# Performance work log

Hardware: AMD Instinct MI355X
Metric: run time of the kernel (lower is better)

## Reference

```python
import jax, jax.numpy as jnp
import numpy as np
from jax import lax

# VGG16 conv configuration: (in_ch, out_ch) for 13 3x3 convs, blocks [2,2,3,3,3]
CONV_CFG = [(3,64),(64,64),(64,128),(128,128),(128,256),(256,256),(256,256),(256,512),(512,512),(512,512),(512,512),(512,512),(512,512)]
FC_CFG = [(512*7*7,4096),(4096,4096),(4096,1000)]
BLOCKS = [2,2,3,3,3]

def setup_inputs() -> dict:
    key = jax.random.key(0)
    ks = jax.random.split(key, 40)
    d = {"x": jax.random.normal(ks[0], (16,3,224,224), jnp.float32)}
    for i, (cin, cout) in enumerate(CONV_CFG):
        std = (2.0 / (cin * 9)) ** 0.5  # He init keeps 13-deep ReLU chain stable
        d[f"w{i+1}"] = jax.random.normal(ks[1+i], (cout, cin, 3, 3), jnp.float32) * std
        d[f"b{i+1}"] = jnp.zeros((cout,), jnp.float32)
    for j, (fin, fout) in enumerate(FC_CFG):
        std = (2.0 / fin) ** 0.5
        d[f"fw{j+1}"] = jax.random.normal(ks[20+j], (fin, fout), jnp.float32) * std
        d[f"fb{j+1}"] = jnp.zeros((fout,), jnp.float32)
    d["patch_location_tensor"] = jax.random.randint(ks[30], (16, 2), 0, 200)
    d["p_height"] = 16
    d["p_width"] = 16
    return d

def _conv_relu(x, w, b):
    # 3x3 conv, stride 1, SAME padding (pad=1), NCHW, followed by ReLU
    y = lax.conv_general_dilated(x, w, (1, 1), 'SAME', dimension_numbers=('NCHW', 'OIHW', 'NCHW'))
    return jax.nn.relu(y + b[None, :, None, None])

def _maxpool2(x):
    return lax.reduce_window(x, -jnp.inf, lax.max, (1, 1, 2, 2), (1, 1, 2, 2), 'VALID')

def reference(x, w1, b1, w2, b2, w3, b3, w4, b4, w5, b5, w6, b6, w7, b7, w8, b8, w9, b9, w10, b10, w11, b11, w12, b12, w13, b13, fw1, fb1, fw2, fb2, fw3, fb3, patch_location_tensor, p_height, p_width):
    # The incremental modules patch-update cached full-model activations; the net
    # result equals a dense VGG16 forward on x. patch_location_tensor / p_height /
    # p_width only control which region is recomputed, not the output values.
    ws = [w1, w2, w3, w4, w5, w6, w7, w8, w9, w10, w11, w12, w13]
    bs = [b1, b2, b3, b4, b5, b6, b7, b8, b9, b10, b11, b12, b13]
    h = x
    k = 0
    for n in BLOCKS:
        for _ in range(n):
            h = _conv_relu(h, ws[k], bs[k])
            k += 1
        h = _maxpool2(h)
    h = h.reshape(h.shape[0], -1)  # [B, 25088]
    h = jax.nn.relu(h @ fw1 + fb1)
    h = jax.nn.relu(h @ fw2 + fb2)
    return h @ fw3 + fb3  # [B, 1000]
```

## Files before the change

### kernel.cpp

```cpp
#include <hip/hip_runtime.h>
#include <hip/hip_bf16.h>

typedef __hip_bfloat16 bf16;
typedef __attribute__((ext_vector_type(4))) short s16x4;
typedef __attribute__((ext_vector_type(8))) short short8;
typedef __attribute__((ext_vector_type(8))) __bf16 bf16x8;
typedef __attribute__((ext_vector_type(4))) float f32x4;

__device__ __forceinline__ float s2f(short s) {
  return __builtin_bit_cast(float, (unsigned)((unsigned short)s) << 16);
}
__device__ __forceinline__ short f2s(float f) {
  return __builtin_bit_cast(short, __float2bfloat16(f));
}

__device__ __forceinline__ void gl16(const bf16* g, bf16* l) {
  __builtin_amdgcn_global_load_lds(
      (const __attribute__((address_space(1))) void*)g,
      (__attribute__((address_space(3))) void*)l, 16, 0, 0);
}

__global__ void zerofill(float* p, int n) {
  int i = blockIdx.x * 256 + threadIdx.x;
  if (i < n) p[i] = 0.f;
}

__global__ __launch_bounds__(256) void conv1_first(
    const float* __restrict__ x, const float* __restrict__ w,
    const float* __restrict__ b, bf16* __restrict__ out) {
  __shared__ float it[3][18][18];
  __shared__ float wl2[27 * 64];
  __shared__ float bl[64];
  const int tid = threadIdx.x;
  const int n = blockIdx.z;
  const int h0 = blockIdx.y * 16, w0 = blockIdx.x * 16;
  for (int i = tid; i < 1728; i += 256) {
    int jj = i >> 6, co = i & 63;
    wl2[i] = w[co * 27 + jj];
  }
  if (tid < 64) bl[tid] = b[tid];
  for (int i = tid; i < 972; i += 256) {
    int ci = i / 324; int r = i - ci * 324; int ty = r / 18, tx = r - ty * 18;
    int hh = h0 - 1 + ty, ww = w0 - 1 + tx;
    float v = 0.f;
    if (hh >= 0 && hh < 224 && ww >= 0 && ww < 224)
      v = x[((long)n * 3 + ci) * 50176 + hh * 224 + ww];
    it[ci][ty][tx] = v;
  }
  __syncthreads();
  const int ty = tid >> 4, tx = tid & 15;
  long ob = (((long)n * 224 + h0 + ty) * 224 + (w0 + tx)) * 64;
  for (int cog = 0; cog < 4; ++cog) {
    f32x4 a4[4];
    #pragma unroll
    for (int q = 0; q < 4; ++q) a4[q] = *(const f32x4*)&bl[cog * 16 + q * 4];
    #pragma unroll
    for (int jj = 0; jj < 27; ++jj) {
      const int ci = jj / 9, r = jj - ci * 9, kh = r / 3, kw = r - kh * 3;
      float v = it[ci][ty + kh][tx + kw];
      const f32x4* wp4 = (const f32x4*)&wl2[jj * 64 + cog * 16];
      #pragma unroll
      for (int q = 0; q < 4; ++q) a4[q] += v * wp4[q];
    }
    short8 s0, s1;
    #pragma unroll
    for (int u = 0; u < 4; ++u) {
      s0[u] = f2s(fmaxf(a4[0][u], 0.f));
      s0[4 + u] = f2s(fmaxf(a4[1][u], 0.f));
      s1[u] = f2s(fmaxf(a4[2][u], 0.f));
      s1[4 + u] = f2s(fmaxf(a4[3][u], 0.f));
    }
    *(short8*)(out + ob + cog * 16) = s0;
    *(short8*)(out + ob + cog * 16 + 8) = s1;
  }
}

struct RepackMeta {
  const float* src[12];
  long dstOff[12];
  int cinM1[12];
  int cshift[12];
  int cout[12];
};

__global__ __launch_bounds__(256) void repack_all(RepackMeta m, bf16* __restrict__ blob) {
  const int li = blockIdx.y;
  const int co = blockIdx.x;
  if (co >= m.cout[li]) return;
  const int cs = m.cshift[li];
  const int cinM1 = m.cinM1[li];
  const int K = 9 << cs;
  const float* src = m.src[li] + (long)co * (cinM1 + 1) * 9;
  bf16* dst = blob + m.dstOff[li] + (long)co * K;
  for (int k = threadIdx.x; k < K; k += 256) {
    int pos = k >> cs;
    int ci = k & cinM1;
    dst[k] = __float2bfloat16(src[ci * 9 + pos]);
  }
}

template <int BM, int BN, int WM, int WN, int SPLITK>
__global__ __launch_bounds__(WM* WN * 64) void conv_gemm(
    const bf16* __restrict__ in, const bf16* __restrict__ wp,
    const float* __restrict__ bias, bf16* __restrict__ out,
    float* __restrict__ pout, const bf16* __restrict__ zp,
    int Cin, int cshift, int Cout, int H, int W, int NHW) {
  constexpr int NT = WM * WN * 64;
  constexpr int IA = BM * 8 / NT;
  constexpr int IB = BN * 8 / NT;
  __shared__ bf16 lA[BM * 64];
  __shared__ bf16 lB[BN * 64];
  const int tid = threadIdx.x;
  const int lane = tid & 63, wv = tid >> 6;
  const int wr = wv / WN, wc = wv % WN;

  const int gx = gridDim.x;
  const int nwg = gx * gridDim.y;
  const int fid = blockIdx.y * gx + blockIdx.x;
  const int q = nwg >> 3, r = nwg & 7;
  const int xcd = fid & 7, idx = fid >> 3;
  const int swz = (xcd < r ? xcd * (q + 1) : r * (q + 1) + (xcd - r) * q) + idx;
  const int p0 = (swz % gx) * BM;
  const int co0 = (swz / gx) * BN;

  const int K = 9 << cshift;
  const int HW = H * W;
  const int colx = ((tid & 7) ^ ((tid >> 3) & 7)) * 8;

  int baseA[IA]; short hA[IA], wA[IA];
  #pragma unroll
  for (int i = 0; i < IA; ++i) {
    int rr = i * (NT / 8) + (tid >> 3);
    int p = p0 + rr;
    if (p < NHW) {
      int n = p / HW; int rem = p - n * HW; int h = rem / W; int w_ = rem - h * W;
      hA[i] = (short)h; wA[i] = (short)w_;
      baseA[i] = ((n * H + h) * W + w_) * Cin;
    } else { hA[i] = -9999; wA[i] = -9999; baseA[i] = 0; }
  }

  f32x4 acc[4][4];
  #pragma unroll
  for (int m = 0; m < 4; ++m)
    #pragma unroll
    for (int n2 = 0; n2 < 4; ++n2) acc[m][n2] = (f32x4){0.f, 0.f, 0.f, 0.f};

  const int Kper = K / SPLITK;
  const int kBeg = (SPLITK > 1) ? (int)blockIdx.z * Kper : 0;
  const int kEnd = kBeg + Kper;

  const bf16* srcB[IB];
  #pragma unroll
  for (int i = 0; i < IB; ++i) {
    int col = i * (NT / 8) + (tid >> 3);
    srcB[i] = wp + (long)(co0 + col) * K + kBeg + colx;
  }

  int kk = kBeg;
  while (kk < kEnd) {
    const int pos = kk >> cshift;
    const int dh = pos / 3 - 1, dw = pos - (pos / 3) * 3 - 1;
    int posEnd = (pos + 1) << cshift;
    if (posEnd > kEnd) posEnd = kEnd;
    const bf16* srcA[IA];
    {
      const int doff = (dh * W + dw) * Cin + (kk & (Cin - 1)) + colx;
      #pragma unroll
      for (int i = 0; i < IA; ++i) {
        int hh = hA[i] + dh, ww = wA[i] + dw;
        bool ok = (hh >= 0) & (hh < H) & (ww >= 0) & (ww < W);
        srcA[i] = ok ? (in + baseA[i] + doff) : (zp + colx);
      }
    }
    for (; kk < posEnd; kk += 64) {
      __syncthreads();
      #pragma unroll
      for (int i = 0; i < IA; ++i) {
        gl16(srcA[i], lA + i * (NT * 8) + wv * 512);
        srcA[i] += 64;
      }
      #pragma unroll
      for (int i = 0; i < IB; ++i) {
        gl16(srcB[i], lB + i * (NT * 8) + wv * 512);
        srcB[i] += 64;
      }
      __syncthreads();
      #pragma unroll
      for (int ks = 0; ks < 2; ++ks) {
        const int kb = ks * 64 + (lane >> 4) * 16;
        bf16x8 af[4], bfv[4];
        #pragma unroll
        for (int m = 0; m < 4; ++m) {
          int rr = wr * 64 + m * 16 + (lane & 15);
          af[m] = *(const bf16x8*)((const char*)lA + rr * 128 + (kb ^ ((rr & 7) << 4)));
        }
        #pragma unroll
        for (int n2 = 0; n2 < 4; ++n2) {
          int c = wc * 64 + n2 * 16 + (lane & 15);
          bfv[n2] = *(const bf16x8*)((const char*)lB + c * 128 + (kb ^ ((c & 7) << 4)));
        }
        #pragma unroll
        for (int m = 0; m < 4; ++m)
          #pragma unroll
          for (int n2 = 0; n2 < 4; ++n2)
            acc[m][n2] = __builtin_amdgcn_mfma_f32_16x16x32_bf16(af[m], bfv[n2], acc[m][n2], 0, 0, 0);
      }
    }
  }

  if constexpr (SPLITK == 1) {
    #pragma unroll
    for (int m = 0; m < 4; ++m) {
      int pb = p0 + wr * 64 + m * 16 + (lane >> 4) * 4;
      #pragma unroll
      for (int n2 = 0; n2 < 4; ++n2) {
        int co = co0 + wc * 64 + n2 * 16 + (lane & 15);
        float bb = bias[co];
        #pragma unroll
        for (int qq = 0; qq < 4; ++qq) {
          int pp = pb + qq;
          if (pp < NHW)
            out[(long)pp * Cout + co] = __float2bfloat16(fmaxf(acc[m][n2][qq] + bb, 0.f));
        }
      }
    }
  } else {
    float* pb_ = pout + (long)blockIdx.z * NHW * Cout;
    #pragma unroll
    for (int m = 0; m < 4; ++m) {
      int pb = p0 + wr * 64 + m * 16 + (lane >> 4) * 4;
      #pragma unroll
      for (int n2 = 0; n2 < 4; ++n2) {
        int co = co0 + wc * 64 + n2 * 16 + (lane & 15);
        #pragma unroll
        for (int qq = 0; qq < 4; ++qq) {
          int pp = pb + qq;
          if (pp < NHW) pb_[(long)pp * Cout + co] = acc[m][n2][qq];
        }
      }
    }
  }
}

template <int NPARTS, bool POOL>
__global__ __launch_bounds__(256) void reduce_split(
    const float* __restrict__ part, const float* __restrict__ bias,
    bf16* __restrict__ out, int NHW, int H, int W, int C) {
  const long total = (long)NHW * C;
  if constexpr (!POOL) {
    long e4 = ((long)blockIdx.x * 256 + threadIdx.x) * 4;
    if (e4 >= total) return;
    f32x4 s = *(const f32x4*)(part + e4);
    #pragma unroll
    for (int p2 = 1; p2 < NPARTS; ++p2) {
      f32x4 b = *(const f32x4*)(part + (long)p2 * total + e4);
      s += b;
    }
    f32x4 bv = *(const f32x4*)(bias + (int)(e4 & (C - 1)));
    s16x4 r;
    #pragma unroll
    for (int u = 0; u < 4; ++u) r[u] = f2s(fmaxf(s[u] + bv[u], 0.f));
    *(s16x4*)(out + e4) = r;
  } else {
    const int H2 = H >> 1, W2 = W >> 1;
    long id4 = ((long)blockIdx.x * 256 + threadIdx.x) * 4;
    long ptotal = ((long)NHW / 4) * C;
    if (id4 >= ptotal) return;
    int c4 = (int)(id4 & (C - 1));
    long rest = id4 / C;
    int wo = (int)(rest % W2);
    long t2 = rest / W2;
    int ho = (int)(t2 % H2);
    int n = (int)(t2 / H2);
    f32x4 bv = *(const f32x4*)(bias + c4);
    f32x4 mx;
    #pragma unroll
    for (int dy = 0; dy < 2; ++dy)
      #pragma unroll
      for (int dx = 0; dx < 2; ++dx) {
        long p = ((long)n * H + 2 * ho + dy) * W + 2 * wo + dx;
        long e = p * C + c4;
        f32x4 s = *(const f32x4*)(part + e);
        #pragma unroll
        for (int p2 = 1; p2 < NPARTS; ++p2) {
          f32x4 b = *(const f32x4*)(part + (long)p2 * total + e);
          s += b;
        }
        s += bv;
        if (dy == 0 && dx == 0) mx = s;
        else {
          #pragma unroll
          for (int u = 0; u < 4; ++u) mx[u] = fmaxf(mx[u], s[u]);
        }
      }
    s16x4 r;
    #pragma unroll
    for (int u = 0; u < 4; ++u) r[u] = f2s(fmaxf(mx[u], 0.f));
    *(s16x4*)(out + ((long)(n * H2 + ho) * W2 + wo) * C + c4) = r;
  }
}

__global__ void maxpool_nhwc(const bf16* __restrict__ in, bf16* __restrict__ out,
                             int H, int W, int C, int cshift3, int WC8) {
  const int id = blockIdx.x * 256 + threadIdx.x;
  if (id >= WC8) return;
  const int H2 = H >> 1, W2 = W >> 1;
  const int ho = blockIdx.y, n = blockIdx.z;
  const int wo = id >> cshift3, c8 = id & ((1 << cshift3) - 1);
  const bf16* p = in + (((long)(n * H + 2 * ho) * W) + 2 * wo) * C + c8 * 8;
  short8 a = *(const short8*)p;
  short8 bq = *(const short8*)(p + C);
  short8 c = *(const short8*)(p + (long)W * C);
  short8 d = *(const short8*)(p + (long)W * C + C);
  short8 r;
  #pragma unroll
  for (int u = 0; u < 8; ++u) {
    float m = fmaxf(fmaxf(s2f(a[u]), s2f(bq[u])), fmaxf(s2f(c[u]), s2f(d[u])));
    r[u] = f2s(m);
  }
  *(short8*)(out + ((long)(n * H2 + ho) * W2 + wo) * C + c8 * 8) = r;
}

__global__ __launch_bounds__(256) void fc1_partial(
    const bf16* __restrict__ in, const float* __restrict__ w,
    float* __restrict__ part) {
  const int j0 = blockIdx.x * 1024 + threadIdx.x * 4;
  const int k0 = blockIdx.y * 128;
  __shared__ float ilds[128][16];
  #pragma unroll
  for (int i = 0; i < 8; ++i) {
    int e = i * 256 + threadIdx.x;
    int kk = e >> 4, n = e & 15;
    int k = k0 + kk;
    int cch = k / 49, s = k - cch * 49;
    ilds[kk][n] = s2f(__builtin_bit_cast(short, in[((long)n * 49 + s) * 512 + cch]));
  }
  __syncthreads();
  f32x4 acc[16];
  #pragma unroll
  for (int n = 0; n < 16; ++n) acc[n] = (f32x4){0.f, 0.f, 0.f, 0.f};
  #pragma unroll 4
  for (int kk = 0; kk < 128; ++kk) {
    f32x4 w4 = *(const f32x4*)(w + (long)(k0 + kk) * 4096 + j0);
    #pragma unroll
    for (int n = 0; n < 16; ++n) {
      float v = ilds[kk][n];
      acc[n] += v * w4;
    }
  }
  float* pp = part + (long)blockIdx.y * 16 * 4096;
  #pragma unroll
  for (int n = 0; n < 16; ++n) *(f32x4*)(pp + n * 4096 + j0) = acc[n];
}

template <int KPER>
__global__ __launch_bounds__(256) void fc23_partial(
    const float* __restrict__ in, const float* __restrict__ w,
    float* __restrict__ part, int fin, int fout) {
  const int j0 = blockIdx.x * 1024 + threadIdx.x * 4;
  const int k0 = blockIdx.y * KPER;
  __shared__ float ilds[KPER][16];
  #pragma unroll
  for (int i = 0; i < KPER / 16; ++i) {
    int e = i * 256 + threadIdx.x;
    int kk = e >> 4, n = e & 15;
    ilds[kk][n] = fmaxf(in[(long)n * fin + k0 + kk], 0.f);
  }
  __syncthreads();
  if (j0 >= fout) return;
  f32x4 acc[16];
  #pragma unroll
  for (int n = 0; n < 16; ++n) acc[n] = (f32x4){0.f, 0.f, 0.f, 0.f};
  #pragma unroll 4
  for (int kk = 0; kk < KPER; ++kk) {
    f32x4 w4 = *(const f32x4*)(w + (long)(k0 + kk) * fout + j0);
    #pragma unroll
    for (int n = 0; n < 16; ++n) {
      float v = ilds[kk][n];
      acc[n] += v * w4;
    }
  }
  float* pp = part + (long)blockIdx.y * 16 * fout;
  #pragma unroll
  for (int n = 0; n < 16; ++n) *(f32x4*)(pp + n * fout + j0) = acc[n];
}

__global__ void reduce_fc(const float* __restrict__ part, const float* __restrict__ bias,
                          float* __restrict__ out, int nparts, int fout, int total) {
  int i = blockIdx.x * 256 + threadIdx.x;
  if (i >= total) return;
  int n = i / fout, j = i - n * fout;
  float s = bias[j];
  for (int p = 0; p < nparts; ++p) s += part[((long)p * 16 + n) * fout + j];
  out[i] = s;
}

extern "C" void kernel_launch(void* const* d_in, const int* in_sizes, int n_in,
                              void* d_out, int out_size, void* d_ws, size_t ws_size,
                              hipStream_t stream) {
  const float* x = (const float*)d_in[0];
  const float* cw[13]; const float* cb[13];
  for (int i = 0; i < 13; ++i) { cw[i] = (const float*)d_in[1 + 2 * i]; cb[i] = (const float*)d_in[2 + 2 * i]; }
  const float* fw1 = (const float*)d_in[27]; const float* fb1 = (const float*)d_in[28];
  const float* fw2 = (const float*)d_in[29]; const float* fb2 = (const float*)d_in[30];
  const float* fw3 = (const float*)d_in[31]; const float* fb3 = (const float*)d_in[32];
  float* outp = (float*)d_out;

  const size_t REGION = 102760448;
  char* wsb = (char*)d_ws;
  bf16* A = (bf16*)wsb;
  bf16* B = (bf16*)(wsb + REGION);
  char* ST = wsb + 2 * REGION;
  bf16* zp = (bf16*)ST;
  bf16* WBLOB = (bf16*)(ST + 4096);
  char* ST2 = ST + 4096 + 31 * 1024 * 1024;
  float* F1 = (float*)ST2;
  float* F2 = F1 + 16 * 4096;
  float* PS = F2 + 16 * 4096;

  struct LayerCfg { int cin, cs, cout, H, W; };
  const LayerCfg L[12] = {
      {64, 6, 64, 224, 224},  {64, 6, 128, 112, 112}, {128, 7, 128, 112, 112},
      {128, 7, 256, 56, 56},  {256, 8, 256, 56, 56},  {256, 8, 256, 56, 56},
      {256, 8, 512, 28, 28},  {512, 9, 512, 28, 28},  {512, 9, 512, 28, 28},
      {512, 9, 512, 14, 14},  {512, 9, 512, 14, 14},  {512, 9, 512, 14, 14}};
  const bool poolAfter[12] = {true, false, true, false, false, true, false, false, true, false, false, true};

  RepackMeta rm;
  long off = 0;
  long offs[12];
  for (int li = 0; li < 12; ++li) {
    rm.src[li] = cw[li + 1];
    rm.cinM1[li] = L[li].cin - 1;
    rm.cshift[li] = L[li].cs;
    rm.cout[li] = L[li].cout;
    rm.dstOff[li] = off;
    offs[li] = off;
    off += (long)L[li].cout * (9 << L[li].cs);
  }
  zerofill<<<4, 256, 0, stream>>>((float*)zp, 1024);
  repack_all<<<dim3(512, 12), 256, 0, stream>>>(rm, WBLOB);

  conv1_first<<<dim3(14, 14, 16), 256, 0, stream>>>(x, cw[0], cb[0], A);

  bf16* cur = A;
  bf16* oth = B;
  for (int li = 0; li < 12; ++li) {
    const LayerCfg& c = L[li];
    bf16* wb = WBLOB + offs[li];
    const int NHW = 16 * c.H * c.W;
    const bool fusedPool = poolAfter[li] && li >= 6;
    if (li == 0) {
      conv_gemm<256, 64, 4, 1, 1><<<dim3(NHW / 256, 1), 256, 0, stream>>>(
          cur, wb, cb[li + 1], oth, nullptr, zp, c.cin, c.cs, c.cout, c.H, c.W, NHW);
    } else if (li <= 2) {
      conv_gemm<128, 128, 2, 2, 1><<<dim3(NHW / 128, c.cout / 128), 256, 0, stream>>>(
          cur, wb, cb[li + 1], oth, nullptr, zp, c.cin, c.cs, c.cout, c.H, c.W, NHW);
    } else if (li <= 5) {
      conv_gemm<128, 256, 2, 4, 1><<<dim3(NHW / 128, 1), 512, 0, stream>>>(
          cur, wb, cb[li + 1], oth, nullptr, zp, c.cin, c.cs, c.cout, c.H, c.W, NHW);
    } else if (li <= 8) {
      conv_gemm<128, 256, 2, 4, 2><<<dim3((NHW + 127) / 128, c.cout / 256, 2), 512, 0, stream>>>(
          cur, wb, cb[li + 1], nullptr, PS, zp, c.cin, c.cs, c.cout, c.H, c.W, NHW);
      if (fusedPool) {
        long pt = ((long)NHW / 4) * c.cout;
        reduce_split<2, true><<<(int)((pt / 4 + 255) / 256), 256, 0, stream>>>(
            PS, cb[li + 1], oth, NHW, c.H, c.W, c.cout);
      } else {
        long tot = (long)NHW * c.cout;
        reduce_split<2, false><<<(int)((tot / 4 + 255) / 256), 256, 0, stream>>>(
            PS, cb[li + 1], oth, NHW, c.H, c.W, c.cout);
      }
    } else {
      conv_gemm<128, 128, 2, 2, 4><<<dim3((NHW + 127) / 128, c.cout / 128, 4), 256, 0, stream>>>(
          cur, wb, cb[li + 1], nullptr, PS, zp, c.cin, c.cs, c.cout, c.H, c.W, NHW);
      if (fusedPool) {
        long pt = ((long)NHW / 4) * c.cout;
        reduce_split<4, true><<<(int)((pt / 4 + 255) / 256), 256, 0, stream>>>(
            PS, cb[li + 1], oth, NHW, c.H, c.W, c.cout);
      } else {
        long tot = (long)NHW * c.cout;
        reduce_split<4, false><<<(int)((tot / 4 + 255) / 256), 256, 0, stream>>>(
            PS, cb[li + 1], oth, NHW, c.H, c.W, c.cout);
      }
    }
    bf16* t = cur; cur = oth; oth = t;
    if (poolAfter[li] && !fusedPool) {
      int cs3 = (c.cout == 64) ? 3 : (c.cout == 128) ? 4 : (c.cout == 256) ? 5 : 6;
      int W2 = c.W / 2, H2 = c.H / 2;
      int WC8 = W2 << cs3;
      maxpool_nhwc<<<dim3((WC8 + 255) / 256, H2, 16), 256, 0, stream>>>(cur, oth, c.H, c.W, c.cout, cs3, WC8);
      t = cur; cur = oth; oth = t;
    }
  }
  float* P1 = (float*)oth;
  float* P2 = (float*)((char*)oth + 52u * 1024 * 1024);
  float* P3 = (float*)((char*)oth + 89u * 1024 * 1024);

  fc1_partial<<<dim3(4, 196), 256, 0, stream>>>(cur, fw1, P1);
  reduce_fc<<<(16 * 4096 + 255) / 256, 256, 0, stream>>>(P1, fb1, F1, 196, 4096, 16 * 4096);
  fc23_partial<32><<<dim3(4, 128), 256, 0, stream>>>(F1, fw2, P2, 4096, 4096);
  reduce_fc<<<(16 * 4096 + 255) / 256, 256, 0, stream>>>(P2, fb2, F2, 128, 4096, 16 * 4096);
  fc23_partial<32><<<dim3(1, 128), 256, 0, stream>>>(F2, fw3, P3, 4096, 1000);
  reduce_fc<<<(16 * 1000 + 255) / 256, 256, 0, stream>>>(P3, fb3, outp, 128, 1000, 16 * 1000);
}
```

Measured before the change: 1.160 ms.

## Add halo-tiled implicit GEMM kernel for 64-channel conv2 layer

Replaces the generic implicit-GEMM path for the second 3x3 conv (64->64 at 224x224) with a dedicated kernel. Each block loads an 8x32 spatial tile plus its halo and all nine weight taps into LDS once, then runs the nine shifted positions from shared memory instead of re-gathering the input for each tap. This cuts redundant global/L2 traffic on the largest layer. In exchange it uses a large LDS footprint (about 117KB per block), which limits occupancy, and it has no pipelining between loads and MFMA.

After: 1.138 ms. No clear change (-1.9%).

```diff
diff --git a/kernel.cpp b/kernel.cpp
--- a/kernel.cpp
+++ b/kernel.cpp
@@ -96,6 +96,93 @@
     int pos = k >> cs;
     int ci = k & cinM1;
     dst[k] = __float2bfloat16(src[ci * 9 + pos]);
+  }
+}
+
+__global__ __launch_bounds__(256) void conv_halo64(
+    const bf16* __restrict__ in, const bf16* __restrict__ wp,
+    const float* __restrict__ bias, bf16* __restrict__ out,
+    const bf16* __restrict__ zp) {
+  __shared__ bf16 tA[10 * 34 * 64];
+  __shared__ bf16 tB[9 * 64 * 64];
+  const int tid = threadIdx.x;
+  const int lane = tid & 63, wv = tid >> 6;
+  const int n = blockIdx.z;
+  const int h0 = blockIdx.y * 8, w0 = blockIdx.x * 32;
+
+  #pragma unroll
+  for (int i = 0; i < 11; ++i) {
+    int cid = i * 256 + tid;
+    if (cid < 2720) {
+      int row = cid / 272;
+      int rem = cid - row * 272;
+      int w = rem >> 3, j = rem & 7;
+      int hg = h0 - 1 + row, wg = w0 - 1 + w;
+      bool ok = (hg >= 0) & (hg < 224) & (wg >= 0) & (wg < 224);
+      const bf16* src = ok ? (in + (((long)n * 224 + hg) * 224 + wg) * 64 + ((j ^ (w & 7)) << 3))
+                           : zp;
+      gl16(src, tA + (long)cid * 8);
+    }
+  }
+  {
+    const int colB = tid >> 3;
+    const int colx = ((tid & 7) ^ (colB & 7)) * 8;
+    const bf16* s0 = wp + (long)colB * 576 + colx;
+    const bf16* s1 = wp + (long)(colB + 32) * 576 + colx;
+    #pragma unroll
+    for (int p = 0; p < 9; ++p) {
+      gl16(s0 + p * 64, tB + p * 4096 + tid * 8);
+      gl16(s1 + p * 64, tB + p * 4096 + 2048 + tid * 8);
+    }
+  }
+  __syncthreads();
+
+  f32x4 acc[4][4];
+  #pragma unroll
+  for (int m = 0; m < 4; ++m)
+    #pragma unroll
+    for (int n2 = 0; n2 < 4; ++n2) acc[m][n2] = (f32x4){0.f, 0.f, 0.f, 0.f};
+
+  for (int pos = 0; pos < 9; ++pos) {
+    const int dh = pos / 3, dw = pos - (pos / 3) * 3;
+    #pragma unroll
+    for (int ks = 0; ks < 2; ++ks) {
+      const int kb = ks * 64 + (lane >> 4) * 16;
+      bf16x8 af[4], bfv[4];
+      #pragma unroll
+      for (int m = 0; m < 4; ++m) {
+        int p = wv * 64 + m * 16 + (lane & 15);
+        int hl = (p >> 5) + dh, wl = (p & 31) + dw;
+        af[m] = *(const bf16x8*)((const char*)tA + hl * 4352 + wl * 128 + (kb ^ ((wl & 7) << 4)));
+      }
+      #pragma unroll
+      for (int n2 = 0; n2 < 4; ++n2) {
+        int c = n2 * 16 + (lane & 15);
+        bfv[n2] = *(const bf16x8*)((const char*)tB + pos * 8192 + c * 128 + (kb ^ ((c & 7) << 4)));
+      }
+      #pragma unroll
+      for (int m = 0; m < 4; ++m)
+        #pragma unroll
+        for (int n2 = 0; n2 < 4; ++n2)
+          acc[m][n2] = __builtin_amdgcn_mfma_f32_16x16x32_bf16(af[m], bfv[n2], acc[m][n2], 0, 0, 0);
+    }
+  }
+
+  #pragma unroll
+  for (int m = 0; m < 4; ++m) {
+    int pbase = wv * 64 + m * 16 + (lane >> 4) * 4;
+    #pragma unroll
+    for (int n2 = 0; n2 < 4; ++n2) {
+      int co = n2 * 16 + (lane & 15);
+      float bb = bias[co];
+      #pragma unroll
+      for (int qq = 0; qq < 4; ++qq) {
+        int p = pbase + qq;
+        int hl = p >> 5, wl = p & 31;
+        out[(((long)n * 224 + h0 + hl) * 224 + (w0 + wl)) * 64 + co] =
+            __float2bfloat16(fmaxf(acc[m][n2][qq] + bb, 0.f));
+      }
+    }
   }
 }
 
@@ -451,8 +538,7 @@
     const int NHW = 16 * c.H * c.W;
     const bool fusedPool = poolAfter[li] && li >= 6;
     if (li == 0) {
-      conv_gemm<256, 64, 4, 1, 1><<<dim3(NHW / 256, 1), 256, 0, stream>>>(
-          cur, wb, cb[li + 1], oth, nullptr, zp, c.cin, c.cs, c.cout, c.H, c.W, NHW);
+      conv_halo64<<<dim3(7, 28, 16), 256, 0, stream>>>(cur, wb, cb[li + 1], oth, zp);
     } else if (li <= 2) {
       conv_gemm<128, 128, 2, 2, 1><<<dim3(NHW / 128, c.cout / 128), 256, 0, stream>>>(
           cur, wb, cb[li + 1], oth, nullptr, zp, c.cin, c.cs, c.cout, c.H, c.W, NHW);
```
